# Kernel tuning notes

Measured on AMD Instinct MI355X. Metric: run time of the kernel, lower is better.

## Reference

```python
import jax, jax.numpy as jnp
import numpy as np

B, H, S, D = 2, 16, 2048, 64

def setup_inputs() -> dict:
    key = jax.random.key(0)
    kq, kk, kv = jax.random.split(key, 3)
    Q = jax.random.normal(kq, (B, H, S, D), dtype=jnp.float32)
    K = jax.random.normal(kk, (B, H, S, D), dtype=jnp.float32)
    V = jax.random.normal(kv, (B, H, S, D), dtype=jnp.float32)
    # causal mask, broadcastable over batch and heads
    mask = jnp.tril(jnp.ones((S, S), dtype=bool))[None, None, :, :]
    return {"Q": Q, "K": K, "V": V, "mask": mask}

def reference(Q, K, V, mask):
    # scores: [B,H,S,S]
    scores = jnp.einsum('bhqd,bhkd->bhqk', Q, K)
    # original applies mask (-inf) BEFORE scaling; -inf/scale == -inf so math matches
    scores = jnp.where(mask, scores, -jnp.inf)
    scores = scores / jnp.sqrt(jnp.float32(K.shape[-1]))
    attn = jax.nn.softmax(scores, axis=-1)
    return jnp.einsum('bhqk,bhkd->bhqd', attn, V)
```

## Files before the change

### kernel.cpp

```cpp
#include <hip/hip_runtime.h>

#define SEQ 2048
#define HD  64
#define SCALE 0.18033688011111772f

typedef __bf16 bf16x8 __attribute__((ext_vector_type(8)));
typedef __bf16 bf16x4 __attribute__((ext_vector_type(4)));
typedef float  f32x4  __attribute__((ext_vector_type(4)));
typedef float  f32x16 __attribute__((ext_vector_type(16)));

__global__ __launch_bounds__(256, 4) void attn_fwd(
    const float* __restrict__ Q,
    const float* __restrict__ K,
    const float* __restrict__ V,
    float* __restrict__ O)
{
    __shared__ __align__(16) unsigned char smem[26624];
    #define KBp(kh,key,c8) ((__bf16*)(smem +         (((kh)<<12) + ((key)<<7) + ((c8)<<4))))
    #define VTp(kh,r,c8)   ((__bf16*)(smem +  8192 + (((kh)<<12) + ((r)<<6)   + ((c8)<<4))))
    #define PWp(w,n,koff)  ((__bf16*)(smem + 16384 + ((w)*2560 + (n)*80 + ((koff)<<1))))

    const int tid   = threadIdx.x;
    const int wave  = tid >> 6;
    const int lane  = tid & 63;
    const int n     = lane & 31;
    const int p     = lane >> 5;
    const int strip = wave & 1;
    const int kh    = wave >> 1;

    const int x  = blockIdx.x;
    const int bh = x & 31;
    const int s  = x >> 5;
    const int q  = (s & 16) ? (31 - (s & 15)) : s;

    const int q0    = q * 64 + strip * 32;
    const int iters = q + 1;
    const int tS0   = kh * (q + 1);

    const float* __restrict__ Qh = Q + (size_t)bh * SEQ * HD;
    const float* __restrict__ Kh = K + (size_t)bh * SEQ * HD;
    const float* __restrict__ Vh = V + (size_t)bh * SEQ * HD;
    float* __restrict__       Oh = O + (size_t)bh * SEQ * HD;

    bf16x8 qf[4];
    {
        const float* qrow = Qh + (size_t)(q0 + n) * HD;
        #pragma unroll
        for (int c = 0; c < 4; ++c) {
            f32x4 a = *(const f32x4*)(qrow + 16 * c + 8 * p);
            f32x4 b = *(const f32x4*)(qrow + 16 * c + 8 * p + 4);
            #pragma unroll
            for (int j = 0; j < 4; ++j) {
                qf[c][j]     = (__bf16)(a[j] * SCALE);
                qf[c][4 + j] = (__bf16)(b[j] * SCALE);
            }
        }
    }

    f32x16 oT[2] = {};
    float  l_own = 0.f;

    const int local = tid & 127;
    const int key_s = local >> 2;
    const int dgi   = local & 3;
    const int Ls    = local & 31;
    const int ko    = local >> 5;
    const int swk   = key_s & 7;
    const int swv   = Ls & 3;

    const float* kbase = Kh + (size_t)key_s * HD + dgi * 16;
    const float* vbase = Vh + (size_t)(ko * 8) * HD + 2 * Ls;

    f32x4  kst[4];
    float2 vst[8];
    {
        const float* kp = kbase + (size_t)(32 * tS0) * HD;
        #pragma unroll
        for (int i = 0; i < 4; ++i) kst[i] = *(const f32x4*)(kp + 4 * i);
        const float* vp = vbase + (size_t)(32 * tS0) * HD;
        #pragma unroll
        for (int i = 0; i < 8; ++i) vst[i] = *(const float2*)(vp + (size_t)i * HD);
    }

    for (int i = 0; i < iters; ++i) {
        __syncthreads();

        {
            bf16x8 w0, w1;
            #pragma unroll
            for (int j = 0; j < 4; ++j) {
                w0[j] = (__bf16)kst[0][j]; w0[4 + j] = (__bf16)kst[1][j];
                w1[j] = (__bf16)kst[2][j]; w1[4 + j] = (__bf16)kst[3][j];
            }
            *(bf16x8*)KBp(kh, key_s, (2 * dgi)     ^ swk) = w0;
            *(bf16x8*)KBp(kh, key_s, (2 * dgi + 1) ^ swk) = w1;

            bf16x8 v0, v1;
            #pragma unroll
            for (int j = 0; j < 8; ++j) { v0[j] = (__bf16)vst[j].x; v1[j] = (__bf16)vst[j].y; }
            *(bf16x8*)VTp(kh, 2 * Ls,     ko ^ swv) = v0;
            *(bf16x8*)VTp(kh, 2 * Ls + 1, ko ^ swv) = v1;
        }

        if (i + 1 < iters) {
            const size_t off = (size_t)(32 * (tS0 + i + 1)) * HD;
            const float* kp = kbase + off;
            #pragma unroll
            for (int j = 0; j < 4; ++j) kst[j] = *(const f32x4*)(kp + 4 * j);
            const float* vp = vbase + off;
            #pragma unroll
            for (int j = 0; j < 8; ++j) vst[j] = *(const float2*)(vp + (size_t)j * HD);
        }

        __syncthreads();

        if (!kh || (i < q + strip)) {
            f32x16 sT = {};
            #pragma unroll
            for (int cc = 0; cc < 4; ++cc) {
                bf16x8 kf = *(const bf16x8*)KBp(kh, n, (2 * cc + p) ^ (n & 7));
                sT = __builtin_amdgcn_mfma_f32_32x32x16_bf16(kf, qf[cc], sT, 0, 0, 0);
            }

            const int  T    = tS0 + i;
            const bool diag = (T == 2 * q + strip);

            float pv[16];
            float ts = 0.f;
            #pragma unroll
            for (int r = 0; r < 16; ++r) {
                float pe = __builtin_amdgcn_exp2f(sT[r]);
                if (diag) {
                    const int kk = (r & 3) + 8 * (r >> 2) + 4 * p;
                    pe = (kk <= n) ? pe : 0.f;
                }
                pv[r] = pe;
                ts += pe;
            }
            l_own += ts;

            #pragma unroll
            for (int m = 0; m < 4; ++m) {
                bf16x4 pk;
                #pragma unroll
                for (int j = 0; j < 4; ++j) pk[j] = (__bf16)pv[4 * m + j];
                *(bf16x4*)PWp(wave, n, 8 * m + 4 * p) = pk;
            }
            bf16x8 pf0 = *(const bf16x8*)PWp(wave, n, 8 * p);
            bf16x8 pf1 = *(const bf16x8*)PWp(wave, n, 16 + 8 * p);

            const int swn = (n >> 1) & 3;
            #pragma unroll
            for (int dg = 0; dg < 2; ++dg) {
                bf16x8 vf0 = *(const bf16x8*)VTp(kh, 32 * dg + n, p ^ swn);
                bf16x8 vf1 = *(const bf16x8*)VTp(kh, 32 * dg + n, (2 + p) ^ swn);
                oT[dg] = __builtin_amdgcn_mfma_f32_32x32x16_bf16(vf0, pf0, oT[dg], 0, 0, 0);
                oT[dg] = __builtin_amdgcn_mfma_f32_32x32x16_bf16(vf1, pf1, oT[dg], 0, 0, 0);
            }
        }
    }

    __syncthreads();
    float* Os = (float*)smem;
    const int cb = strip * 2112;
    float l_part = l_own + __shfl_xor(l_own, 32, 64);

    if (kh == 1) {
        #pragma unroll
        for (int dg = 0; dg < 2; ++dg)
            #pragma unroll
            for (int r = 0; r < 16; ++r)
                Os[cb + (dg * 16 + r) * 64 + lane] = oT[dg][r];
        Os[cb + 2048 + lane] = l_part;
    }
    __syncthreads();
    if (kh == 0) {
        const float linv = 1.0f / (l_part + Os[cb + 2048 + lane]);
        #pragma unroll
        for (int dg = 0; dg < 2; ++dg) {
            #pragma unroll
            for (int u = 0; u < 4; ++u) {
                f32x4 o;
                #pragma unroll
                for (int j = 0; j < 4; ++j) {
                    const int r = 4 * u + j;
                    o[j] = (oT[dg][r] + Os[cb + (dg * 16 + r) * 64 + lane]) * linv;
                }
                *(f32x4*)&Oh[(size_t)(q0 + n) * HD + dg * 32 + u * 8 + 4 * p] = o;
            }
        }
    }
}

extern "C" void kernel_launch(void* const* d_in, const int* in_sizes, int n_in,
                              void* d_out, int out_size, void* d_ws, size_t ws_size,
                              hipStream_t stream) {
    const float* Q = (const float*)d_in[0];
    const float* K = (const float*)d_in[1];
    const float* V = (const float*)d_in[2];
    float* O = (float*)d_out;

    dim3 grid(1024);
    dim3 block(256);
    attn_fwd<<<grid, block, 0, stream>>>(Q, K, V, O);
}
```

Before: 132.7 us.

## Pre-convert K/V to bf16 in a separate kernel and read fragments from global

Adds a pre-pass kernel that converts K to bf16 and V to transposed bf16 in the workspace. The attention kernel then loads MFMA fragments straight from global memory (expected to hit L2) instead of staging them through LDS. This removes the per-tile fp32-to-bf16 conversion, the LDS staging and both block-wide barriers, and lets each wave run its own trip count. The trade-off is an extra kernel launch, additional global traffic for the converted copies, and non-prefetched global loads in the inner loop, whose latency now has to be hidden by occupancy.

```diff
diff --git a/kernel.cpp b/kernel.cpp
--- a/kernel.cpp
+++ b/kernel.cpp
@@ -9,16 +9,60 @@
 typedef float  f32x4  __attribute__((ext_vector_type(4)));
 typedef float  f32x16 __attribute__((ext_vector_type(16)));
 
+__global__ __launch_bounds__(256) void cvt_kv(
+    const float* __restrict__ K, const float* __restrict__ V,
+    __bf16* __restrict__ Kw, __bf16* __restrict__ Vt)
+{
+    const int b   = blockIdx.x;
+    const int bh  = b & 31;
+    const int key0 = (b >> 5) * 64;
+    const int t   = threadIdx.x;
+
+    const float* Kh  = K  + (size_t)bh * SEQ * HD;
+    const float* Vh  = V  + (size_t)bh * SEQ * HD;
+    __bf16*      Kwh = Kw + (size_t)bh * SEQ * HD;
+    __bf16*      Vth = Vt + (size_t)bh * SEQ * HD;
+
+    {
+        const int key = key0 + (t >> 2);
+        const int dc  = (t & 3) * 16;
+        const float* kp = Kh + (size_t)key * HD + dc;
+        f32x4 a0 = *(const f32x4*)(kp);
+        f32x4 a1 = *(const f32x4*)(kp + 4);
+        f32x4 a2 = *(const f32x4*)(kp + 8);
+        f32x4 a3 = *(const f32x4*)(kp + 12);
+        bf16x8 w0, w1;
+        #pragma unroll
+        for (int j = 0; j < 4; ++j) {
+            w0[j] = (__bf16)a0[j]; w0[4 + j] = (__bf16)a1[j];
+            w1[j] = (__bf16)a2[j]; w1[4 + j] = (__bf16)a3[j];
+        }
+        *(bf16x8*)(Kwh + (size_t)key * HD + dc)     = w0;
+        *(bf16x8*)(Kwh + (size_t)key * HD + dc + 8) = w1;
+    }
+    {
+        const int Ls = t & 31;
+        const int ko = t >> 5;
+        const float* vp = Vh + (size_t)(key0 + ko * 8) * HD + 2 * Ls;
+        float2 v[8];
+        #pragma unroll
+        for (int j = 0; j < 8; ++j) v[j] = *(const float2*)(vp + (size_t)j * HD);
+        bf16x8 v0, v1;
+        #pragma unroll
+        for (int j = 0; j < 8; ++j) { v0[j] = (__bf16)v[j].x; v1[j] = (__bf16)v[j].y; }
+        *(bf16x8*)(Vth + (size_t)(2 * Ls)     * SEQ + key0 + ko * 8) = v0;
+        *(bf16x8*)(Vth + (size_t)(2 * Ls + 1) * SEQ + key0 + ko * 8) = v1;
+    }
+}
+
 __global__ __launch_bounds__(256, 4) void attn_fwd(
     const float* __restrict__ Q,
-    const float* __restrict__ K,
-    const float* __restrict__ V,
+    const __bf16* __restrict__ Kw,
+    const __bf16* __restrict__ Vt,
     float* __restrict__ O)
 {
-    __shared__ __align__(16) unsigned char smem[26624];
-    #define KBp(kh,key,c8) ((__bf16*)(smem +         (((kh)<<12) + ((key)<<7) + ((c8)<<4))))
-    #define VTp(kh,r,c8)   ((__bf16*)(smem +  8192 + (((kh)<<12) + ((r)<<6)   + ((c8)<<4))))
-    #define PWp(w,n,koff)  ((__bf16*)(smem + 16384 + ((w)*2560 + (n)*80 + ((koff)<<1))))
+    __shared__ __align__(16) unsigned char smem[16896];
+    #define PWp(w,n,koff) ((__bf16*)(smem + ((w)*2560 + (n)*80 + ((koff)<<1))))
 
     const int tid   = threadIdx.x;
     const int wave  = tid >> 6;
@@ -34,13 +78,13 @@
     const int q  = (s & 16) ? (31 - (s & 15)) : s;
 
     const int q0    = q * 64 + strip * 32;
-    const int iters = q + 1;
     const int tS0   = kh * (q + 1);
+    const int nIter = kh ? (q + strip) : (q + 1);
 
-    const float* __restrict__ Qh = Q + (size_t)bh * SEQ * HD;
-    const float* __restrict__ Kh = K + (size_t)bh * SEQ * HD;
-    const float* __restrict__ Vh = V + (size_t)bh * SEQ * HD;
-    float* __restrict__       Oh = O + (size_t)bh * SEQ * HD;
+    const float*  __restrict__ Qh  = Q  + (size_t)bh * SEQ * HD;
+    const __bf16* __restrict__ Kwh = Kw + (size_t)bh * SEQ * HD;
+    const __bf16* __restrict__ Vth = Vt + (size_t)bh * SEQ * HD;
+    float* __restrict__        Oh  = O  + (size_t)bh * SEQ * HD;
 
     bf16x8 qf[4];
     {
@@ -60,103 +104,50 @@
     f32x16 oT[2] = {};
     float  l_own = 0.f;
 
-    const int local = tid & 127;
-    const int key_s = local >> 2;
-    const int dgi   = local & 3;
-    const int Ls    = local & 31;
-    const int ko    = local >> 5;
-    const int swk   = key_s & 7;
-    const int swv   = Ls & 3;
+    for (int i = 0; i < nIter; ++i) {
+        const int T  = tS0 + i;
+        const int k0 = T * 32;
 
-    const float* kbase = Kh + (size_t)key_s * HD + dgi * 16;
-    const float* vbase = Vh + (size_t)(ko * 8) * HD + 2 * Ls;
-
-    f32x4  kst[4];
-    float2 vst[8];
-    {
-        const float* kp = kbase + (size_t)(32 * tS0) * HD;
+        f32x16 sT = {};
+        const __bf16* krow = Kwh + (size_t)(k0 + n) * HD + 8 * p;
         #pragma unroll
-        for (int i = 0; i < 4; ++i) kst[i] = *(const f32x4*)(kp + 4 * i);
-        const float* vp = vbase + (size_t)(32 * tS0) * HD;
-        #pragma unroll
-        for (int i = 0; i < 8; ++i) vst[i] = *(const float2*)(vp + (size_t)i * HD);
-    }
-
-    for (int i = 0; i < iters; ++i) {
-        __syncthreads();
-
-        {
-            bf16x8 w0, w1;
-            #pragma unroll
-            for (int j = 0; j < 4; ++j) {
-                w0[j] = (__bf16)kst[0][j]; w0[4 + j] = (__bf16)kst[1][j];
-                w1[j] = (__bf16)kst[2][j]; w1[4 + j] = (__bf16)kst[3][j];
-            }
-            *(bf16x8*)KBp(kh, key_s, (2 * dgi)     ^ swk) = w0;
-            *(bf16x8*)KBp(kh, key_s, (2 * dgi + 1) ^ swk) = w1;
-
-            bf16x8 v0, v1;
-            #pragma unroll
-            for (int j = 0; j < 8; ++j) { v0[j] = (__bf16)vst[j].x; v1[j] = (__bf16)vst[j].y; }
-            *(bf16x8*)VTp(kh, 2 * Ls,     ko ^ swv) = v0;
-            *(bf16x8*)VTp(kh, 2 * Ls + 1, ko ^ swv) = v1;
+        for (int c = 0; c < 4; ++c) {
+            bf16x8 kf = *(const bf16x8*)(krow + 16 * c);
+            sT = __builtin_amdgcn_mfma_f32_32x32x16_bf16(kf, qf[c], sT, 0, 0, 0);
         }
 
-        if (i + 1 < iters) {
-            const size_t off = (size_t)(32 * (tS0 + i + 1)) * HD;
-            const float* kp = kbase + off;
+        const bool diag = (T == 2 * q + strip);
+        float pv[16];
+        float ts = 0.f;
+        #pragma unroll
+        for (int r = 0; r < 16; ++r) {
+            float pe = __builtin_amdgcn_exp2f(sT[r]);
+            if (diag) {
+                const int kk = (r & 3) + 8 * (r >> 2) + 4 * p;
+                pe = (kk <= n) ? pe : 0.f;
+            }
+            pv[r] = pe;
+            ts += pe;
+        }
+        l_own += ts;
+
+        #pragma unroll
+        for (int m = 0; m < 4; ++m) {
+            bf16x4 pk;
             #pragma unroll
-            for (int j = 0; j < 4; ++j) kst[j] = *(const f32x4*)(kp + 4 * j);
-            const float* vp = vbase + off;
-            #pragma unroll
-            for (int j = 0; j < 8; ++j) vst[j] = *(const float2*)(vp + (size_t)j * HD);
+            for (int j = 0; j < 4; ++j) pk[j] = (__bf16)pv[4 * m + j];
+            *(bf16x4*)PWp(wave, n, 8 * m + 4 * p) = pk;
         }
+        bf16x8 pf0 = *(const bf16x8*)PWp(wave, n, 8 * p);
+        bf16x8 pf1 = *(const bf16x8*)PWp(wave, n, 16 + 8 * p);
 
-        __syncthreads();
-
-        if (!kh || (i < q + strip)) {
-            f32x16 sT = {};
-            #pragma unroll
-            for (int cc = 0; cc < 4; ++cc) {
-                bf16x8 kf = *(const bf16x8*)KBp(kh, n, (2 * cc + p) ^ (n & 7));
-                sT = __builtin_amdgcn_mfma_f32_32x32x16_bf16(kf, qf[cc], sT, 0, 0, 0);
-            }
-
-            const int  T    = tS0 + i;
-            const bool diag = (T == 2 * q + strip);
-
-            float pv[16];
-            float ts = 0.f;
-            #pragma unroll
-            for (int r = 0; r < 16; ++r) {
-                float pe = __builtin_amdgcn_exp2f(sT[r]);
-                if (diag) {
-                    const int kk = (r & 3) + 8 * (r >> 2) + 4 * p;
-                    pe = (kk <= n) ? pe : 0.f;
-                }
-                pv[r] = pe;
-                ts += pe;
-            }
-            l_own += ts;
-
-            #pragma unroll
-            for (int m = 0; m < 4; ++m) {
-                bf16x4 pk;
-                #pragma unroll
-                for (int j = 0; j < 4; ++j) pk[j] = (__bf16)pv[4 * m + j];
-                *(bf16x4*)PWp(wave, n, 8 * m + 4 * p) = pk;
-            }
-            bf16x8 pf0 = *(const bf16x8*)PWp(wave, n, 8 * p);
-            bf16x8 pf1 = *(const bf16x8*)PWp(wave, n, 16 + 8 * p);
-
-            const int swn = (n >> 1) & 3;
-            #pragma unroll
-            for (int dg = 0; dg < 2; ++dg) {
-                bf16x8 vf0 = *(const bf16x8*)VTp(kh, 32 * dg + n, p ^ swn);
-                bf16x8 vf1 = *(const bf16x8*)VTp(kh, 32 * dg + n, (2 + p) ^ swn);
-                oT[dg] = __builtin_amdgcn_mfma_f32_32x32x16_bf16(vf0, pf0, oT[dg], 0, 0, 0);
-                oT[dg] = __builtin_amdgcn_mfma_f32_32x32x16_bf16(vf1, pf1, oT[dg], 0, 0, 0);
-            }
+        const __bf16* vrow = Vth + (size_t)n * SEQ + k0 + 8 * p;
+        #pragma unroll
+        for (int dg = 0; dg < 2; ++dg) {
+            bf16x8 vf0 = *(const bf16x8*)(vrow + (size_t)(32 * dg) * SEQ);
+            bf16x8 vf1 = *(const bf16x8*)(vrow + (size_t)(32 * dg) * SEQ + 16);
+            oT[dg] = __builtin_amdgcn_mfma_f32_32x32x16_bf16(vf0, pf0, oT[dg], 0, 0, 0);
+            oT[dg] = __builtin_amdgcn_mfma_f32_32x32x16_bf16(vf1, pf1, oT[dg], 0, 0, 0);
         }
     }
 
@@ -200,7 +191,9 @@
     const float* V = (const float*)d_in[2];
     float* O = (float*)d_out;
 
-    dim3 grid(1024);
-    dim3 block(256);
-    attn_fwd<<<grid, block, 0, stream>>>(Q, K, V, O);
+    __bf16* Kw = (__bf16*)d_ws;
+    __bf16* Vt = (__bf16*)((unsigned char*)d_ws + (8u << 20));
+
+    cvt_kv<<<dim3(1024), dim3(256), 0, stream>>>(K, V, Kw, Vt);
+    attn_fwd<<<dim3(1024), dim3(256), 0, stream>>>(Q, Kw, Vt, O);
 }
```

New measurement: 170.7 us. 28.7% more time.
